# Optimization experiments

Measured on AMD Instinct MI355X. Metric: run time of the kernel, lower is better.

Reference implementation:

```python
import jax, jax.numpy as jnp
import numpy as np

NH, HD = 16, 64
STRIDE = 8
TOP_K_PCT = 0.1
NEG = -1e9


def setup_inputs() -> dict:
    key = jax.random.key(0)
    ks = jax.random.split(key, 6)
    B, T, D = 1, 2048, 1024
    x = jax.random.normal(ks[0], (B, T, D), dtype=jnp.float32)
    U = jax.random.uniform(ks[1], (B, T), dtype=jnp.float32)
    s = 1.0 / np.sqrt(D)
    wq = jax.random.normal(ks[2], (NH * HD, D), dtype=jnp.float32) * s
    wk = jax.random.normal(ks[3], (NH * HD, D), dtype=jnp.float32) * s
    wv = jax.random.normal(ks[4], (NH * HD, D), dtype=jnp.float32) * s
    wo = jax.random.normal(ks[5], (D, NH * HD), dtype=jnp.float32) * s
    return {"x": x, "U": U, "wq": wq, "wk": wk, "wv": wv, "wo": wo}


def _derive_mask(Q, K, U, T):
    # downsampled scores: [B, nH, T/8, T/8]
    Qd = Q[:, :, ::STRIDE, :]
    Kd = K[:, :, ::STRIDE, :]
    scores = jnp.einsum('bhid,bhjd->bhij', Qd, Kd) * (HD ** -0.5)
    # upsample back to [B, nH, T, T] via repeat_interleave
    sf = jnp.repeat(jnp.repeat(scores, STRIDE, axis=2), STRIDE, axis=3)[:, :, :T, :T]
    u_scale = (1.0 + jnp.clip(U, 0.0, 1.0))[:, None, :, None]  # [B,1,T,1]
    sf = sf * u_scale
    k = max(1, int(T * TOP_K_PCT))
    kth = jax.lax.top_k(sf, k)[0][..., k - 1:k]  # kth-largest per row, [B,nH,T,1]
    return jax.nn.sigmoid((sf - kth) * 10.0)


def reference(x, U, wq, wk, wv, wo):
    B, T, D = x.shape
    Q = (x @ wq.T).reshape(B, T, NH, HD).transpose(0, 2, 1, 3)
    K = (x @ wk.T).reshape(B, T, NH, HD).transpose(0, 2, 1, 3)
    V = (x @ wv.T).reshape(B, T, NH, HD).transpose(0, 2, 1, 3)
    mask = _derive_mask(Q, K, U, T)
    causal = jnp.tril(jnp.ones((T, T), dtype=jnp.float32))
    mask = mask * causal[None, None, :, :]
    scores = jnp.einsum('bhid,bhjd->bhij', Q, K) * (HD ** -0.5)
    scores = scores + (1.0 - mask) * NEG
    attn = jax.nn.softmax(scores, axis=-1)
    out = jnp.einsum('bhij,bhjd->bhid', attn, V)
    out = out.transpose(0, 2, 1, 3).reshape(B, T, NH * HD)
    return out @ wo.T
```

## Files before the change

### kernel.cpp

```cpp
#include <hip/hip_runtime.h>
#include <hip/hip_bf16.h>
#include <cmath>

typedef __attribute__((ext_vector_type(8))) short bf16x8;
typedef __attribute__((ext_vector_type(4))) short bf16x4;
typedef __attribute__((ext_vector_type(4))) float f32x4;

constexpr int Tq  = 2048;
constexpr int Dm  = 1024;
constexpr int NHC = 16;
constexpr int HDC = 64;
constexpr int TDC = 256;
constexpr int KSEL = 26;
constexpr int CH  = 8;

__device__ inline ushort f2bf(float x) {
  union { float f; unsigned u; } v; v.f = x;
  return (ushort)((v.u + 0x7FFF + ((v.u >> 16) & 1)) >> 16);
}
__device__ inline float bf2f(ushort b) {
  union { unsigned u; float f; } v; v.u = ((unsigned)b) << 16;
  return v.f;
}
__device__ inline void gload16(const ushort* g, ushort* l) {
  __builtin_amdgcn_global_load_lds(
      (const __attribute__((address_space(1))) unsigned int*)g,
      (__attribute__((address_space(3))) unsigned int*)l, 16, 0, 0);
}

__global__ __launch_bounds__(256) void cast_split_all(
    const float* __restrict__ x,  const float* __restrict__ wq,
    const float* __restrict__ wk, const float* __restrict__ wv,
    const float* __restrict__ wo,
    ushort* __restrict__ xh,  ushort* __restrict__ xl,
    ushort* __restrict__ wqh, ushort* __restrict__ wql,
    ushort* __restrict__ wkh, ushort* __restrict__ wkl,
    ushort* __restrict__ wvh, ushort* __restrict__ wvl,
    ushort* __restrict__ woh, ushort* __restrict__ wol) {
  int bid = blockIdx.x;
  const float* src; ushort *hi, *lo; int blk;
  if (bid < 2048)      { src = x;  hi = xh;  lo = xl;  blk = bid; }
  else {
    int z = (bid - 2048) >> 10;
    blk = (bid - 2048) & 1023;
    if (z == 0)      { src = wq; hi = wqh; lo = wql; }
    else if (z == 1) { src = wk; hi = wkh; lo = wkl; }
    else if (z == 2) { src = wv; hi = wvh; lo = wvl; }
    else             { src = wo; hi = woh; lo = wol; }
  }
  int base = (blk * 256 + threadIdx.x) * 4;
  float4 v = *(const float4*)&src[base];
  ushort h0 = f2bf(v.x), h1 = f2bf(v.y), h2 = f2bf(v.z), h3 = f2bf(v.w);
  *(ushort4*)&hi[base] = make_ushort4(h0, h1, h2, h3);
  *(ushort4*)&lo[base] = make_ushort4(
      f2bf(v.x - bf2f(h0)), f2bf(v.y - bf2f(h1)),
      f2bf(v.z - bf2f(h2)), f2bf(v.w - bf2f(h3)));
}

__global__ __launch_bounds__(256, 2) void fused_gemms(
    const float* __restrict__ x, const float* __restrict__ wq,
    const float* __restrict__ wk, float* __restrict__ Qd,
    float* __restrict__ Kd, float* __restrict__ xp,
    const ushort* __restrict__ xh_, const ushort* __restrict__ xl_,
    const ushort* __restrict__ wqh_, const ushort* __restrict__ wql_,
    const ushort* __restrict__ wkh_, const ushort* __restrict__ wkl_,
    const ushort* __restrict__ wvh_, const ushort* __restrict__ wvl_,
    ushort* __restrict__ Qh, ushort* __restrict__ Ql,
    ushort* __restrict__ Kh, ushort* __restrict__ Kl,
    ushort* __restrict__ Vth) {
  __shared__ __align__(16) char smem[65536];
  int bid = blockIdx.x;
  int tid = threadIdx.x;
  if (bid < 128) {
    int mat = bid >> 6;
    int rem = bid & 63;
    int n0 = (rem & 15) * 64, m0 = (rem >> 4) * 64;
    const float* B = mat ? wk : wq;
    float* C = mat ? Kd : Qd;
    typedef float lds16x68[16][68];
    lds16x68* As = (lds16x68*)(smem);
    lds16x68* Bs = (lds16x68*)(smem + 2 * 16 * 68 * 4);
    int tx = tid & 15, ty = tid >> 4;
    int srow = tid >> 2, sc4 = tid & 3;
    const float* Arow = &x[(size_t)((m0 + srow) * 8) * 1024 + sc4 * 4];
    const float* Brow = &B[(size_t)(n0 + srow) * 1024 + sc4 * 4];
    float acc[4][4] = {};
    {
      float4 av = *(const float4*)&Arow[0];
      float4 bv = *(const float4*)&Brow[0];
      As[0][sc4 * 4 + 0][srow] = av.x; As[0][sc4 * 4 + 1][srow] = av.y;
      As[0][sc4 * 4 + 2][srow] = av.z; As[0][sc4 * 4 + 3][srow] = av.w;
      Bs[0][sc4 * 4 + 0][srow] = bv.x; Bs[0][sc4 * 4 + 1][srow] = bv.y;
      Bs[0][sc4 * 4 + 2][srow] = bv.z; Bs[0][sc4 * 4 + 3][srow] = bv.w;
    }
    __syncthreads();
    for (int iter = 0; iter < 64; ++iter) {
      int cbuf = iter & 1, nbuf = cbuf ^ 1;
      bool hn = (iter + 1 < 64);
      float4 av, bv;
      if (hn) {
        int k0 = (iter + 1) * 16;
        av = *(const float4*)&Arow[k0];
        bv = *(const float4*)&Brow[k0];
      }
#pragma unroll
      for (int k = 0; k < 16; ++k) {
        float a[4], b[4];
#pragma unroll
        for (int i = 0; i < 4; ++i) {
          a[i] = As[cbuf][k][ty * 4 + i];
          b[i] = Bs[cbuf][k][tx * 4 + i];
        }
#pragma unroll
        for (int i = 0; i < 4; ++i)
#pragma unroll
          for (int j = 0; j < 4; ++j) acc[i][j] += a[i] * b[j];
      }
      if (hn) {
        As[nbuf][sc4 * 4 + 0][srow] = av.x; As[nbuf][sc4 * 4 + 1][srow] = av.y;
        As[nbuf][sc4 * 4 + 2][srow] = av.z; As[nbuf][sc4 * 4 + 3][srow] = av.w;
        Bs[nbuf][sc4 * 4 + 0][srow] = bv.x; Bs[nbuf][sc4 * 4 + 1][srow] = bv.y;
        Bs[nbuf][sc4 * 4 + 2][srow] = bv.z; Bs[nbuf][sc4 * 4 + 3][srow] = bv.w;
      }
      __syncthreads();
    }
#pragma unroll
    for (int i = 0; i < 4; ++i)
#pragma unroll
      for (int j = 0; j < 4; ++j)
        C[(size_t)(m0 + ty * 4 + i) * 1024 + n0 + tx * 4 + j] = acc[i][j];
    return;
  }
  if (bid < 192) {
    int b = bid - 128;
    float4 s = {0.f, 0.f, 0.f, 0.f};
    for (int r = 0; r < 32; ++r) {
      float4 v = *(const float4*)&x[(size_t)(b * 32 + r) * Dm + tid * 4];
      s.x += v.x; s.y += v.y; s.z += v.z; s.w += v.w;
    }
    *(float4*)&xp[b * Dm + tid * 4] = s;
    return;
  }
  int q_ = bid - 192;
  int z = q_ >> 7, rem = q_ & 127;
  int n0 = (rem & 7) * 128, m0 = (rem >> 3) * 128;
  const ushort* Bhp = (z == 0) ? wqh_ : ((z == 1) ? wkh_ : wvh_);
  const ushort* Blp = (z == 0) ? wql_ : ((z == 1) ? wkl_ : wvl_);
  ushort (*AhS)[64] = (ushort(*)[64])(smem);
  ushort (*AlS)[64] = (ushort(*)[64])(smem + 16384);
  ushort (*BhS)[64] = (ushort(*)[64])(smem + 32768);
  ushort (*BlS)[64] = (ushort(*)[64])(smem + 49152);
  int w = tid >> 6, l = tid & 63, l15 = l & 15, lg = l >> 4;
  int qr = w >> 1, qc = w & 1;
  int lrow = l >> 3, lc8 = l & 7;
  f32x4 acc[4][4] = {};
  for (int k0 = 0; k0 < Dm; k0 += 64) {
    __syncthreads();
#pragma unroll
    for (int s = 0; s < 4; ++s) {
      int row = 32 * w + s * 8 + lrow;
      int scol = (lc8 ^ (row & 7)) * 8;
      size_t ao = (size_t)(m0 + row) * Dm + k0 + scol;
      size_t bo = (size_t)(n0 + row) * Dm + k0 + scol;
      gload16(&xh_[ao], &AhS[32 * w + s * 8][0]);
      gload16(&xl_[ao], &AlS[32 * w + s * 8][0]);
      gload16(&Bhp[bo], &BhS[32 * w + s * 8][0]);
      gload16(&Blp[bo], &BlS[32 * w + s * 8][0]);
    }
    __syncthreads();
#pragma unroll
    for (int kst = 0; kst < 2; ++kst) {
      bf16x8 ah[4], al[4], bh[4], bl[4];
#pragma unroll
      for (int i = 0; i < 4; ++i) {
        int ar = qr * 64 + i * 16 + l15;
        int sa = ((kst * 4 + lg) ^ (ar & 7)) * 8;
        ah[i] = *(const bf16x8*)&AhS[ar][sa];
        al[i] = *(const bf16x8*)&AlS[ar][sa];
        int br = qc * 64 + i * 16 + l15;
        int sb = ((kst * 4 + lg) ^ (br & 7)) * 8;
        bh[i] = *(const bf16x8*)&BhS[br][sb];
        bl[i] = *(const bf16x8*)&BlS[br][sb];
      }
#pragma unroll
      for (int i = 0; i < 4; ++i)
#pragma unroll
        for (int j = 0; j < 4; ++j) {
          acc[i][j] = __builtin_amdgcn_mfma_f32_16x16x32_bf16(ah[i], bh[j], acc[i][j], 0, 0, 0);
          acc[i][j] = __builtin_amdgcn_mfma_f32_16x16x32_bf16(al[i], bh[j], acc[i][j], 0, 0, 0);
          acc[i][j] = __builtin_amdgcn_mfma_f32_16x16x32_bf16(ah[i], bl[j], acc[i][j], 0, 0, 0);
        }
    }
  }
#pragma unroll
  for (int i = 0; i < 4; ++i)
#pragma unroll
    for (int j = 0; j < 4; ++j) {
      int r0 = m0 + qr * 64 + i * 16 + lg * 4;
      int cc = n0 + qc * 64 + j * 16 + l15;
      if (z <= 1) {
        ushort* Chi = (z == 0) ? Qh : Kh;
        ushort* Clo = (z == 0) ? Ql : Kl;
        size_t o = (size_t)(cc >> 6) * Tq * HDC + (size_t)r0 * HDC + (cc & 63);
#pragma unroll
        for (int rg = 0; rg < 4; ++rg) {
          float v = acc[i][j][rg];
          ushort hh = f2bf(v);
          Chi[o + (size_t)rg * HDC] = hh;
          Clo[o + (size_t)rg * HDC] = f2bf(v - bf2f(hh));
        }
      } else {
        bf16x4 ph;
#pragma unroll
        for (int rg = 0; rg < 4; ++rg) ph[rg] = (short)f2bf(acc[i][j][rg]);
        size_t o = (size_t)(cc >> 6) * HDC * Tq + (size_t)(cc & 63) * Tq + r0;
        *(bf16x4*)&Vth[o] = ph;
      }
    }
}

__global__ __launch_bounds__(256, 2) void gemm128_out(
    const ushort* __restrict__ Ah, const ushort* __restrict__ Al,
    const ushort* __restrict__ Bh, const ushort* __restrict__ Bl,
    float* __restrict__ Cf) {
  __shared__ ushort AhS[128][64], AlS[128][64], BhS[128][64], BlS[128][64];
  int tid = threadIdx.x, w = tid >> 6, l = tid & 63, l15 = l & 15, lg = l >> 4;
  int qr = w >> 1, qc = w & 1;
  int lrow = l >> 3, lc8 = l & 7;
  int m0 = blockIdx.y * 128, n0 = blockIdx.x * 128;
  f32x4 acc[4][4] = {};
  for (int k0 = 0; k0 < Dm; k0 += 64) {
    __syncthreads();
#pragma unroll
    for (int s = 0; s < 4; ++s) {
      int row = 32 * w + s * 8 + lrow;
      int scol = (lc8 ^ (row & 7)) * 8;
      size_t ao = (size_t)(m0 + row) * Dm + k0 + scol;
      size_t bo = (size_t)(n0 + row) * Dm + k0 + scol;
      gload16(&Ah[ao], &AhS[32 * w + s * 8][0]);
      gload16(&Al[ao], &AlS[32 * w + s * 8][0]);
      gload16(&Bh[bo], &BhS[32 * w + s * 8][0]);
      gload16(&Bl[bo], &BlS[32 * w + s * 8][0]);
    }
    __syncthreads();
#pragma unroll
    for (int kst = 0; kst < 2; ++kst) {
      bf16x8 ah[4], al[4], bh[4], bl[4];
#pragma unroll
      for (int i = 0; i < 4; ++i) {
        int ar = qr * 64 + i * 16 + l15;
        int sa = ((kst * 4 + lg) ^ (ar & 7)) * 8;
        ah[i] = *(const bf16x8*)&AhS[ar][sa];
        al[i] = *(const bf16x8*)&AlS[ar][sa];
        int br = qc * 64 + i * 16 + l15;
        int sb = ((kst * 4 + lg) ^ (br & 7)) * 8;
        bh[i] = *(const bf16x8*)&BhS[br][sb];
        bl[i] = *(const bf16x8*)&BlS[br][sb];
      }
#pragma unroll
      for (int i = 0; i < 4; ++i)
#pragma unroll
        for (int j = 0; j < 4; ++j) {
          acc[i][j] = __builtin_amdgcn_mfma_f32_16x16x32_bf16(ah[i], bh[j], acc[i][j], 0, 0, 0);
          acc[i][j] = __builtin_amdgcn_mfma_f32_16x16x32_bf16(al[i], bh[j], acc[i][j], 0, 0, 0);
          acc[i][j] = __builtin_amdgcn_mfma_f32_16x16x32_bf16(ah[i], bl[j], acc[i][j], 0, 0, 0);
        }
    }
  }
#pragma unroll
  for (int i = 0; i < 4; ++i)
#pragma unroll
    for (int j = 0; j < 4; ++j) {
      int r0 = m0 + qr * 64 + i * 16 + lg * 4;
      int cc = n0 + qc * 64 + j * 16 + l15;
#pragma unroll
      for (int rg = 0; rg < 4; ++rg)
        Cf[(size_t)(r0 + rg) * Dm + cc] = acc[i][j][rg];
    }
}

__global__ __launch_bounds__(256) void sd_kernel(
    const float* __restrict__ Qd, const float* __restrict__ Kd,
    float* __restrict__ Sd) {
  __shared__ float Qs[64][68];
  __shared__ float Ks[64][68];
  int jk0 = blockIdx.x * 64, iq0 = blockIdx.y * 64, h = blockIdx.z;
  int tid = threadIdx.x, tx = tid & 15, ty = tid >> 4;
#pragma unroll
  for (int q = 0; q < 4; ++q) {
    int f = tid * 4 + q;
    int row = f >> 4, c4 = f & 15;
    float4 q4 = *(const float4*)&Qd[(size_t)(iq0 + row) * Dm + h * HDC + c4 * 4];
    float4 k4 = *(const float4*)&Kd[(size_t)(jk0 + row) * Dm + h * HDC + c4 * 4];
    Qs[c4 * 4 + 0][row] = q4.x; Qs[c4 * 4 + 1][row] = q4.y;
    Qs[c4 * 4 + 2][row] = q4.z; Qs[c4 * 4 + 3][row] = q4.w;
    Ks[c4 * 4 + 0][row] = k4.x; Ks[c4 * 4 + 1][row] = k4.y;
    Ks[c4 * 4 + 2][row] = k4.z; Ks[c4 * 4 + 3][row] = k4.w;
  }
  __syncthreads();
  float acc[4][4] = {};
#pragma unroll
  for (int k = 0; k < 64; ++k) {
    float a[4], b[4];
#pragma unroll
    for (int i = 0; i < 4; ++i) { a[i] = Qs[k][ty * 4 + i]; b[i] = Ks[k][tx * 4 + i]; }
#pragma unroll
    for (int i = 0; i < 4; ++i)
#pragma unroll
      for (int j = 0; j < 4; ++j) acc[i][j] += a[i] * b[j];
  }
#pragma unroll
  for (int i = 0; i < 4; ++i)
#pragma unroll
    for (int j = 0; j < 4; ++j)
      Sd[(size_t)(h * TDC + iq0 + ty * 4 + i) * TDC + jk0 + tx * 4 + j] =
          acc[i][j] * 0.125f;
}

__global__ __launch_bounds__(256) void fused_kth_xm(
    const float* __restrict__ Sd, float* __restrict__ kth,
    const float* __restrict__ xp, float* __restrict__ xm) {
  int blk = blockIdx.x, tid = threadIdx.x;
  if (blk < 1024) {
    int lane = tid & 63;
    int b = blk * 4 + (tid >> 6);
    const float* row = &Sd[(size_t)b * TDC];
    float v[4];
#pragma unroll
    for (int j = 0; j < 4; ++j) v[j] = row[lane + 64 * j];
    float ans = 0.f;
    for (int it = 0; it < KSEL; ++it) {
      float lm = fmaxf(fmaxf(v[0], v[1]), fmaxf(v[2], v[3]));
#pragma unroll
      for (int off = 1; off < 64; off <<= 1) lm = fmaxf(lm, __shfl_xor(lm, off));
      if (it == KSEL - 1) { ans = lm; break; }
      unsigned long long ball =
          __ballot(v[0] == lm || v[1] == lm || v[2] == lm || v[3] == lm);
      int first = __ffsll(ball) - 1;
      if (lane == first) {
        if (v[0] == lm) v[0] = -INFINITY;
        else if (v[1] == lm) v[1] = -INFINITY;
        else if (v[2] == lm) v[2] = -INFINITY;
        else v[3] = -INFINITY;
      }
    }
    if (lane == 0) kth[b] = ans;
  } else {
    float4 s = {0.f, 0.f, 0.f, 0.f};
    for (int i = 0; i < 64; ++i) {
      float4 v = *(const float4*)&xp[i * Dm + tid * 4];
      s.x += v.x; s.y += v.y; s.z += v.z; s.w += v.w;
    }
    float4 o = {s.x * (1.f / 2048.f), s.y * (1.f / 2048.f),
                s.z * (1.f / 2048.f), s.w * (1.f / 2048.f)};
    *(float4*)&xm[tid * 4] = o;
  }
}

__global__ __launch_bounds__(256) void fused_attn_vm(
    const ushort* __restrict__ Qh, const ushort* __restrict__ Ql,
    const ushort* __restrict__ Kh, const ushort* __restrict__ Kl,
    const ushort* __restrict__ Vth, const float* __restrict__ U,
    const float* __restrict__ Sd, const float* __restrict__ kth,
    const float* __restrict__ xm, const float* __restrict__ wv,
    float* __restrict__ Vm,
    ushort* __restrict__ Pacc, float* __restrict__ Pm, float* __restrict__ Pl) {
  int pidx = blockIdx.x;
  int tid = threadIdx.x;
  if (pidx >= 1280) {
    int h = pidx - 1280;
    int r = h * 64 + (tid >> 2), q = tid & 3;
    const float* wrow = wv + (size_t)r * Dm + q * 256;
    const float* a = xm + q * 256;
    float s = 0.f;
    for (int k = 0; k < 256; k += 4) {
      float4 w4 = *(const float4*)&wrow[k];
      float4 a4 = *(const float4*)&a[k];
      s += w4.x * a4.x + w4.y * a4.y + w4.z * a4.z + w4.w * a4.w;
    }
    s += __shfl_xor(s, 1); s += __shfl_xor(s, 2);
    if (q == 0) Vm[r] = s;
    return;
  }
  int xcd = pidx & 7, idx = pidx >> 3;
  int h = xcd * 2 + (idx & 1);
  int p = idx >> 1;
  int c, qt;
  if (p < 32)      { c = 0; qt = p; }
  else if (p < 56) { c = 1; qt = p - 24; }
  else if (p < 72) { c = 2; qt = p - 40; }
  else             { c = 3; qt = p - 48; }
  int w = tid >> 6, l = tid & 63, l15 = l & 15, lg = l >> 4;
  int lrow = l >> 3, lc8 = l & 7;
  int i0 = qt * 64;
  int irow = i0 + 16 * w + l15;

  __shared__ ushort KhS[64][64], KlS[64][64], VhS[64][64];
  __shared__ ushort Ps[4][16][72];

  float uu; { float t = U[irow]; uu = 1.f + fminf(fmaxf(t, 0.f), 1.f); }
  int i8 = irow >> 3;
  float kv = kth[h * TDC + i8];
  float kvu = kv * uu;
  const float* SdRow = Sd + ((size_t)h * TDC + i8) * TDC;

  size_t qoff = ((size_t)h * Tq + irow) * HDC;
  bf16x8 qh0 = *(const bf16x8*)(Qh + qoff + lg * 8);
  bf16x8 qh1 = *(const bf16x8*)(Qh + qoff + 32 + lg * 8);
  bf16x8 ql0 = *(const bf16x8*)(Ql + qoff + lg * 8);
  bf16x8 ql1 = *(const bf16x8*)(Ql + qoff + 32 + lg * 8);

  float mrow = -INFINITY, lrow_acc = 0.f;
  f32x4 acc[4] = {};

  int jt1 = min(c * CH + CH, qt + 1);
  for (int jt = c * CH; jt < jt1; ++jt) {
    int j0 = jt * 64;
    __syncthreads();
#pragma unroll
    for (int hh = 0; hh < 2; ++hh) {
      int row = 16 * w + hh * 8 + lrow;
      int scol = (lc8 ^ (row & 7)) * 8;
      size_t ko = ((size_t)h * Tq + j0 + row) * HDC + scol;
      size_t vo = ((size_t)h * HDC + row) * Tq + j0 + scol;
      gload16(&Kh[ko], &KhS[16 * w + hh * 8][0]);
      gload16(&Kl[ko], &KlS[16 * w + hh * 8][0]);
      gload16(&Vth[vo], &VhS[16 * w + hh * 8][0]);
    }

    float pen[4];
    {
      int jb0 = (j0 >> 3) + (lg >> 1);
#pragma unroll
      for (int nt = 0; nt < 4; ++nt) {
        float sdv = SdRow[jb0 + nt * 2];
        float arg = (sdv * uu - kvu) * 10.f;
        float mk;
        if (arg >= 0.f) mk = 1.f / (1.f + expf(-arg));
        else { float e = expf(arg); mk = e / (1.f + e); }
        pen[nt] = (1.f - mk) * (-1.0e9f);
      }
    }
    __syncthreads();

    f32x4 s[4] = {};
#pragma unroll
    for (int nt = 0; nt < 4; ++nt) {
      int kr = nt * 16 + l15;
      int s0 = ((0 + lg) ^ (kr & 7)) * 8;
      int s1 = ((4 + lg) ^ (kr & 7)) * 8;
      bf16x8 ah0 = *(const bf16x8*)&KhS[kr][s0];
      bf16x8 ah1 = *(const bf16x8*)&KhS[kr][s1];
      bf16x8 al0 = *(const bf16x8*)&KlS[kr][s0];
      bf16x8 al1 = *(const bf16x8*)&KlS[kr][s1];
      s[nt] = __builtin_amdgcn_mfma_f32_16x16x32_bf16(ah0, qh0, s[nt], 0, 0, 0);
      s[nt] = __builtin_amdgcn_mfma_f32_16x16x32_bf16(ah1, qh1, s[nt], 0, 0, 0);
      s[nt] = __builtin_amdgcn_mfma_f32_16x16x32_bf16(al0, qh0, s[nt], 0, 0, 0);
      s[nt] = __builtin_amdgcn_mfma_f32_16x16x32_bf16(al1, qh1, s[nt], 0, 0, 0);
      s[nt] = __builtin_amdgcn_mfma_f32_16x16x32_bf16(ah0, ql0, s[nt], 0, 0, 0);
      s[nt] = __builtin_amdgcn_mfma_f32_16x16x32_bf16(ah1, ql1, s[nt], 0, 0, 0);
    }

    bool diag = (jt == qt);
    float lgv[4][4];
    float tmax = -INFINITY;
    if (diag) {
#pragma unroll
      for (int nt = 0; nt < 4; ++nt)
#pragma unroll
        for (int rg = 0; rg < 4; ++rg) {
          int jj = j0 + nt * 16 + lg * 4 + rg;
          float lv = s[nt][rg] * 0.125f + ((jj > irow) ? -1.0e9f : pen[nt]);
          lgv[nt][rg] = lv;
          tmax = fmaxf(tmax, lv);
        }
    } else {
#pragma unroll
      for (int nt = 0; nt < 4; ++nt)
#pragma unroll
        for (int rg = 0; rg < 4; ++rg) {
          float lv = s[nt][rg] * 0.125f + pen[nt];
          lgv[nt][rg] = lv;
          tmax = fmaxf(tmax, lv);
        }
    }
    tmax = fmaxf(tmax, __shfl_xor(tmax, 16));
    tmax = fmaxf(tmax, __shfl_xor(tmax, 32));
    float mnew = fmaxf(mrow, tmax);
    float ps = 0.f;
#pragma unroll
    for (int nt = 0; nt < 4; ++nt) {
      float p0 = __expf(lgv[nt][0] - mnew);
      float p1 = __expf(lgv[nt][1] - mnew);
      float p2 = __expf(lgv[nt][2] - mnew);
      float p3 = __expf(lgv[nt][3] - mnew);
      ps += (p0 + p1) + (p2 + p3);
      uint2 pk;
      asm("v_cvt_pk_bf16_f32 %0, %1, %2" : "=v"(pk.x) : "v"(p0), "v"(p1));
      asm("v_cvt_pk_bf16_f32 %0, %1, %2" : "=v"(pk.y) : "v"(p2), "v"(p3));
      *(uint2*)&Ps[w][l15][nt * 16 + lg * 4] = pk;
    }
    ps += __shfl_xor(ps, 16);
    ps += __shfl_xor(ps, 32);
    if (!__all(tmax <= mrow)) {
      float sc = __expf(mrow - mnew);
      lrow_acc = lrow_acc * sc + ps;
      mrow = mnew;
      float scr[4];
#pragma unroll
      for (int rg = 0; rg < 4; ++rg) scr[rg] = __shfl(sc, lg * 4 + rg);
#pragma unroll
      for (int ntd = 0; ntd < 4; ++ntd)
#pragma unroll
        for (int rg = 0; rg < 4; ++rg) acc[ntd][rg] *= scr[rg];
    } else {
      lrow_acc += ps;
    }

#pragma unroll
    for (int kst = 0; kst < 2; ++kst) {
      bf16x8 pa = *(const bf16x8*)&Ps[w][l15][kst * 32 + lg * 8];
#pragma unroll
      for (int ntd = 0; ntd < 4; ++ntd) {
        int vr = ntd * 16 + l15;
        int sv = ((kst * 4 + lg) ^ (vr & 7)) * 8;
        bf16x8 vbh = *(const bf16x8*)&VhS[vr][sv];
        acc[ntd] = __builtin_amdgcn_mfma_f32_16x16x32_bf16(pa, vbh, acc[ntd], 0, 0, 0);
      }
    }
  }

  size_t rowbase = ((size_t)c * NHC + h) * Tq + i0 + 16 * w;
  if (lg == 0) {
    Pm[rowbase + l15] = mrow;
    Pl[rowbase + l15] = lrow_acc;
  }
#pragma unroll
  for (int ntd = 0; ntd < 4; ++ntd)
#pragma unroll
    for (int rg = 0; rg < 4; ++rg)
      Pacc[(rowbase + lg * 4 + rg) * HDC + ntd * 16 + l15] = f2bf(acc[ntd][rg]);
}

__global__ __launch_bounds__(256) void attn_merge(
    const ushort* __restrict__ Pacc, const float* __restrict__ Pm,
    const float* __restrict__ Pl, const float* __restrict__ Vm,
    ushort* __restrict__ AOh, ushort* __restrict__ AOl) {
  int qt = blockIdx.x, h = blockIdx.y;
  int tid = threadIdx.x;
  int r = tid >> 2, q4 = tid & 3;
  int gi = qt * 64 + r;
  int nc = (qt >> 3) + 1;
  float M = -INFINITY, mv[4];
#pragma unroll
  for (int cc = 0; cc < 4; ++cc) {
    mv[cc] = (cc < nc) ? Pm[((size_t)cc * NHC + h) * Tq + gi] : -INFINITY;
    M = fmaxf(M, mv[cc]);
  }
  if (M == -1.0e9f) {
#pragma unroll
    for (int dd = 0; dd < 16; dd += 4) {
      int d = q4 * 16 + dd;
      float4 v = *(const float4*)&Vm[h * HDC + d];
      float vv[4] = {v.x, v.y, v.z, v.w};
      ushort4 uh, ul;
      ushort* uhp = &uh.x; ushort* ulp = &ul.x;
#pragma unroll
      for (int j = 0; j < 4; ++j) {
        ushort hh = f2bf(vv[j]);
        uhp[j] = hh; ulp[j] = f2bf(vv[j] - bf2f(hh));
      }
      *(ushort4*)&AOh[(size_t)gi * Dm + h * HDC + d] = uh;
      *(ushort4*)&AOl[(size_t)gi * Dm + h * HDC + d] = ul;
    }
    return;
  }
  float W[4], L = 0.f;
#pragma unroll
  for (int cc = 0; cc < 4; ++cc) {
    W[cc] = (cc < nc) ? __expf(mv[cc] - M) : 0.f;
    if (cc < nc) L += Pl[((size_t)cc * NHC + h) * Tq + gi] * W[cc];
  }
  float invL = 1.f / L;
#pragma unroll
  for (int dd = 0; dd < 16; dd += 4) {
    int d = q4 * 16 + dd;
    float o[4] = {0.f, 0.f, 0.f, 0.f};
    for (int cc = 0; cc < nc; ++cc) {
      bf16x4 a = *(const bf16x4*)&Pacc[(((size_t)cc * NHC + h) * Tq + gi) * HDC + d];
#pragma unroll
      for (int j = 0; j < 4; ++j) o[j] += bf2f((ushort)a[j]) * W[cc];
    }
    ushort4 uh, ul;
    ushort* uhp = &uh.x; ushort* ulp = &ul.x;
#pragma unroll
    for (int j = 0; j < 4; ++j) {
      float vv = o[j] * invL;
      ushort hh = f2bf(vv);
      uhp[j] = hh; ulp[j] = f2bf(vv - bf2f(hh));
    }
    *(ushort4*)&AOh[(size_t)gi * Dm + h * HDC + d] = uh;
    *(ushort4*)&AOl[(size_t)gi * Dm + h * HDC + d] = ul;
  }
}

extern "C" void kernel_launch(void* const* d_in, const int* in_sizes, int n_in,
                              void* d_out, int out_size, void* d_ws, size_t ws_size,
                              hipStream_t stream) {
  const float* x  = (const float*)d_in[0];
  const float* U  = (const float*)d_in[1];
  const float* wq = (const float*)d_in[2];
  const float* wk = (const float*)d_in[3];
  const float* wv = (const float*)d_in[4];
  const float* wo = (const float*)d_in[5];
  float* out = (float*)d_out;

  float* fw = (float*)d_ws;
  const size_t TD_ = (size_t)Tq * Dm;
  const size_t WW_ = (size_t)Dm * Dm;
  const size_t QD_ = (size_t)TDC * Dm;
  float* Qd  = fw;                 fw += QD_;
  float* Kd  = fw;                 fw += QD_;
  float* Sd  = fw;                 fw += (size_t)NHC * TDC * TDC;
  float* kth = fw;                 fw += 4096;
  float* Vm  = fw;                 fw += 4096;
  float* xm  = fw;                 fw += 4096;
  float* xp  = fw;                 fw += 64 * Dm;
  float* Pm  = fw;                 fw += 4 * NHC * Tq;
  float* Pl  = fw;                 fw += 4 * NHC * Tq;
  ushort* uw = (ushort*)fw;
  ushort* xh   = uw;               uw += TD_;
  ushort* xl   = uw;               uw += TD_;
  ushort* wqh  = uw;               uw += WW_;
  ushort* wql  = uw;               uw += WW_;
  ushort* wkh  = uw;               uw += WW_;
  ushort* wkl  = uw;               uw += WW_;
  ushort* wvh  = uw;               uw += WW_;
  ushort* wvl  = uw;               uw += WW_;
  ushort* woh  = uw;               uw += WW_;
  ushort* wol  = uw;               uw += WW_;
  ushort* Qh   = uw;               uw += TD_;
  ushort* Ql   = uw;               uw += TD_;
  ushort* Kh   = uw;               uw += TD_;
  ushort* Kl   = uw;               uw += TD_;
  ushort* Vth  = uw;               uw += TD_;
  ushort* Pacc = uw;               uw += (size_t)4 * NHC * Tq * HDC;
  ushort* AOh = xh;
  ushort* AOl = xl;

  dim3 bb(256);
  cast_split_all<<<dim3(6144), bb, 0, stream>>>(
      x, wq, wk, wv, wo, xh, xl, wqh, wql, wkh, wkl, wvh, wvl, woh, wol);
  fused_gemms<<<dim3(576), bb, 0, stream>>>(
      x, wq, wk, Qd, Kd, xp,
      xh, xl, wqh, wql, wkh, wkl, wvh, wvl, Qh, Ql, Kh, Kl, Vth);
  sd_kernel<<<dim3(4, 4, NHC), bb, 0, stream>>>(Qd, Kd, Sd);
  fused_kth_xm<<<dim3(1025), bb, 0, stream>>>(Sd, kth, xp, xm);
  fused_attn_vm<<<dim3(1296), bb, 0, stream>>>(
      Qh, Ql, Kh, Kl, Vth, U, Sd, kth, xm, wv, Vm, Pacc, Pm, Pl);
  attn_merge<<<dim3(Tq / 64, NHC), bb, 0, stream>>>(Pacc, Pm, Pl, Vm, AOh, AOl);
  gemm128_out<<<dim3(8, 16), bb, 0, stream>>>(AOh, AOl, woh, wol, out);
}
```

Before: 181.9 us.

## Fold xp reduction into small GEMM blocks, XCD-aware QKV mapping, smaller out-GEMM tiles

The x row-sum pooling (xp) no longer gets its own 64 blocks. The first 64 downsampled-GEMM blocks do it after their tile, which cuts the fused launch from 576 to 512 blocks. The 384 QKV GEMM blocks are remapped so consecutive block IDs, which go round-robin across the 8 XCDs, land on tiles sharing a weight panel, aiming for better L2 reuse. The output projection now uses 128x64 tiles with 512 threads on a 16x16 grid (256 blocks instead of 128), so it fills more CUs. The cost is a longer tail on some fused blocks and less reuse per tile in the output GEMM.

```diff
diff --git a/kernel.cpp b/kernel.cpp
--- a/kernel.cpp
+++ b/kernel.cpp
@@ -129,21 +129,23 @@
 #pragma unroll
       for (int j = 0; j < 4; ++j)
         C[(size_t)(m0 + ty * 4 + i) * 1024 + n0 + tx * 4 + j] = acc[i][j];
+    if (bid < 64) {
+      int b = bid;
+      float4 s = {0.f, 0.f, 0.f, 0.f};
+      for (int r = 0; r < 32; ++r) {
+        float4 v = *(const float4*)&x[(size_t)(b * 32 + r) * Dm + tid * 4];
+        s.x += v.x; s.y += v.y; s.z += v.z; s.w += v.w;
+      }
+      *(float4*)&xp[b * Dm + tid * 4] = s;
+    }
     return;
   }
-  if (bid < 192) {
-    int b = bid - 128;
-    float4 s = {0.f, 0.f, 0.f, 0.f};
-    for (int r = 0; r < 32; ++r) {
-      float4 v = *(const float4*)&x[(size_t)(b * 32 + r) * Dm + tid * 4];
-      s.x += v.x; s.y += v.y; s.z += v.z; s.w += v.w;
-    }
-    *(float4*)&xp[b * Dm + tid * 4] = s;
-    return;
-  }
-  int q_ = bid - 192;
-  int z = q_ >> 7, rem = q_ & 127;
-  int n0 = (rem & 7) * 128, m0 = (rem >> 3) * 128;
+  int q_ = bid - 128;
+  int xcd = q_ & 7, j_ = q_ >> 3;
+  int panel = xcd * 3 + (j_ >> 4);
+  int m_t = j_ & 15;
+  int z = panel >> 3, n_t = panel & 7;
+  int n0 = n_t * 128, m0 = m_t * 128;
   const ushort* Bhp = (z == 0) ? wqh_ : ((z == 1) ? wkh_ : wvh_);
   const ushort* Blp = (z == 0) ? wql_ : ((z == 1) ? wkl_ : wvl_);
   ushort (*AhS)[64] = (ushort(*)[64])(smem);
@@ -219,48 +221,51 @@
     }
 }
 
-__global__ __launch_bounds__(256, 2) void gemm128_out(
+__global__ __launch_bounds__(512) void gemm_out(
     const ushort* __restrict__ Ah, const ushort* __restrict__ Al,
     const ushort* __restrict__ Bh, const ushort* __restrict__ Bl,
     float* __restrict__ Cf) {
-  __shared__ ushort AhS[128][64], AlS[128][64], BhS[128][64], BlS[128][64];
-  int tid = threadIdx.x, w = tid >> 6, l = tid & 63, l15 = l & 15, lg = l >> 4;
-  int qr = w >> 1, qc = w & 1;
+  __shared__ ushort AhS[128][64], AlS[128][64], BhS[64][64], BlS[64][64];
+  int tid = threadIdx.x;
+  int w = tid >> 6, l = tid & 63, l15 = l & 15, lg = l >> 4;
+  int wr = w >> 1, wc = w & 1;
   int lrow = l >> 3, lc8 = l & 7;
-  int m0 = blockIdx.y * 128, n0 = blockIdx.x * 128;
-  f32x4 acc[4][4] = {};
+  int m0 = blockIdx.y * 128, n0 = blockIdx.x * 64;
+  f32x4 acc[2][2] = {};
   for (int k0 = 0; k0 < Dm; k0 += 64) {
     __syncthreads();
 #pragma unroll
-    for (int s = 0; s < 4; ++s) {
-      int row = 32 * w + s * 8 + lrow;
-      int scol = (lc8 ^ (row & 7)) * 8;
-      size_t ao = (size_t)(m0 + row) * Dm + k0 + scol;
-      size_t bo = (size_t)(n0 + row) * Dm + k0 + scol;
-      gload16(&Ah[ao], &AhS[32 * w + s * 8][0]);
-      gload16(&Al[ao], &AlS[32 * w + s * 8][0]);
-      gload16(&Bh[bo], &BhS[32 * w + s * 8][0]);
-      gload16(&Bl[bo], &BlS[32 * w + s * 8][0]);
+    for (int hh = 0; hh < 2; ++hh) {
+      int row = 16 * w + hh * 8 + lrow;
+      size_t ao = (size_t)(m0 + row) * Dm + k0 + ((lc8 ^ (row & 7)) * 8);
+      gload16(&Ah[ao], &AhS[16 * w + hh * 8][0]);
+      gload16(&Al[ao], &AlS[16 * w + hh * 8][0]);
+    }
+    {
+      int row = 8 * w + lrow;
+      size_t bo = (size_t)(n0 + row) * Dm + k0 + ((lc8 ^ (row & 7)) * 8);
+      gload16(&Bh[bo], &BhS[8 * w][0]);
+      gload16(&Bl[bo], &BlS[8 * w][0]);
     }
     __syncthreads();
 #pragma unroll
     for (int kst = 0; kst < 2; ++kst) {
-      bf16x8 ah[4], al[4], bh[4], bl[4];
-#pragma unroll
-      for (int i = 0; i < 4; ++i) {
-        int ar = qr * 64 + i * 16 + l15;
+      bf16x8 ah[2], al[2], bh[2], bl[2];
+#pragma unroll
+      for (int i = 0; i < 2; ++i) {
+        int ar = wr * 32 + i * 16 + l15;
         int sa = ((kst * 4 + lg) ^ (ar & 7)) * 8;
         ah[i] = *(const bf16x8*)&AhS[ar][sa];
         al[i] = *(const bf16x8*)&AlS[ar][sa];
-        int br = qc * 64 + i * 16 + l15;
+        int br = wc * 32 + i * 16 + l15;
         int sb = ((kst * 4 + lg) ^ (br & 7)) * 8;
         bh[i] = *(const bf16x8*)&BhS[br][sb];
         bl[i] = *(const bf16x8*)&BlS[br][sb];
       }
 #pragma unroll
-      for (int i = 0; i < 4; ++i)
-#pragma unroll
-        for (int j = 0; j < 4; ++j) {
+      for (int i = 0; i < 2; ++i)
+#pragma unroll
+        for (int j = 0; j < 2; ++j) {
           acc[i][j] = __builtin_amdgcn_mfma_f32_16x16x32_bf16(ah[i], bh[j], acc[i][j], 0, 0, 0);
           acc[i][j] = __builtin_amdgcn_mfma_f32_16x16x32_bf16(al[i], bh[j], acc[i][j], 0, 0, 0);
           acc[i][j] = __builtin_amdgcn_mfma_f32_16x16x32_bf16(ah[i], bl[j], acc[i][j], 0, 0, 0);
@@ -268,11 +273,11 @@
     }
   }
 #pragma unroll
-  for (int i = 0; i < 4; ++i)
-#pragma unroll
-    for (int j = 0; j < 4; ++j) {
-      int r0 = m0 + qr * 64 + i * 16 + lg * 4;
-      int cc = n0 + qc * 64 + j * 16 + l15;
+  for (int i = 0; i < 2; ++i)
+#pragma unroll
+    for (int j = 0; j < 2; ++j) {
+      int r0 = m0 + wr * 32 + i * 16 + lg * 4;
+      int cc = n0 + wc * 32 + j * 16 + l15;
 #pragma unroll
       for (int rg = 0; rg < 4; ++rg)
         Cf[(size_t)(r0 + rg) * Dm + cc] = acc[i][j][rg];
@@ -651,7 +656,7 @@
   dim3 bb(256);
   cast_split_all<<<dim3(6144), bb, 0, stream>>>(
       x, wq, wk, wv, wo, xh, xl, wqh, wql, wkh, wkl, wvh, wvl, woh, wol);
-  fused_gemms<<<dim3(576), bb, 0, stream>>>(
+  fused_gemms<<<dim3(512), bb, 0, stream>>>(
       x, wq, wk, Qd, Kd, xp,
       xh, xl, wqh, wql, wkh, wkl, wvh, wvl, Qh, Ql, Kh, Kl, Vth);
   sd_kernel<<<dim3(4, 4, NHC), bb, 0, stream>>>(Qd, Kd, Sd);
@@ -659,5 +664,5 @@
   fused_attn_vm<<<dim3(1296), bb, 0, stream>>>(
       Qh, Ql, Kh, Kl, Vth, U, Sd, kth, xm, wv, Vm, Pacc, Pm, Pl);
   attn_merge<<<dim3(Tq / 64, NHC), bb, 0, stream>>>(Pacc, Pm, Pl, Vm, AOh, AOl);
-  gemm128_out<<<dim3(8, 16), bb, 0, stream>>>(AOh, AOl, woh, wol, out);
-}
+  gemm_out<<<dim3(16, 16), dim3(512), 0, stream>>>(AOh, AOl, woh, wol, out);
+}
```

New measurement: 176.0 us. 3.3% less time.
